# Kernel tuning notes

Measured on AMD Instinct MI355X. Metric: run time of the kernel, lower is better.

The kernel has to match this reference:

```python
import jax, jax.numpy as jnp
import numpy as np

B, T, V, D, H, DK = 64, 384, 12, 256, 4, 64

def _ln(x, g, b):
    m = jnp.mean(x, -1, keepdims=True)
    v = jnp.var(x, -1, keepdims=True)
    return (x - m) * jax.lax.rsqrt(v + 1e-5) * g + b

def _grn(x, W1, b1, W2, b2, Wg, bg, lng, lnb, ctx=None, Wc=None, Ws=None, bs=None):
    # eta2 = ELU(fc1(x) + ctx_proj(ctx)); eta1 = fc2(eta2); GLU; residual; LN
    h = x @ W1 + b1
    if ctx is not None:
        h = h + ctx @ Wc
    h = jax.nn.elu(h)
    h = h @ W2 + b2
    g = h @ Wg + bg
    a, gate = jnp.split(g, 2, axis=-1)
    gated = a * jax.nn.sigmoid(gate)
    skip = x if Ws is None else x @ Ws + bs
    return _ln(skip + gated, lng, lnb)

def setup_inputs() -> dict:
    key = jax.random.key(0)
    ks = iter(jax.random.split(key, 48))
    def rn(shape, s=0.02):
        return jax.random.normal(next(ks), shape, jnp.float32) * s
    return {
        'x': jax.random.normal(next(ks), (B, T, V, D), jnp.float32),
        'context': jax.random.normal(next(ks), (B, D), jnp.float32),
        # flattened GRN of VSN: in=V*D, hidden=D, out=V, context=D, skip needed
        'fg_W1': rn((V * D, D)), 'fg_b1': jnp.zeros((D,), jnp.float32),
        'fg_Wc': rn((D, D)),
        'fg_W2': rn((D, D)), 'fg_b2': jnp.zeros((D,), jnp.float32),
        'fg_Wg': rn((D, 2 * V)), 'fg_bg': jnp.zeros((2 * V,), jnp.float32),
        'fg_Ws': rn((V * D, V)), 'fg_bs': jnp.zeros((V,), jnp.float32),
        'fg_lng': jnp.ones((V,), jnp.float32), 'fg_lnb': jnp.zeros((V,), jnp.float32),
        # per-variable GRNs (V of them, in=out=hidden=D, no skip/ctx), stacked
        'sv_W1': rn((V, D, D)), 'sv_b1': jnp.zeros((V, D), jnp.float32),
        'sv_W2': rn((V, D, D)), 'sv_b2': jnp.zeros((V, D), jnp.float32),
        'sv_Wg': rn((V, D, 2 * D)), 'sv_bg': jnp.zeros((V, 2 * D), jnp.float32),
        'sv_lng': jnp.ones((V, D), jnp.float32), 'sv_lnb': jnp.zeros((V, D), jnp.float32),
        # static enrichment GRN: in=out=hidden=D with context
        'en_W1': rn((D, D)), 'en_b1': jnp.zeros((D,), jnp.float32),
        'en_Wc': rn((D, D)),
        'en_W2': rn((D, D)), 'en_b2': jnp.zeros((D,), jnp.float32),
        'en_Wg': rn((D, 2 * D)), 'en_bg': jnp.zeros((2 * D,), jnp.float32),
        'en_lng': jnp.ones((D,), jnp.float32), 'en_lnb': jnp.zeros((D,), jnp.float32),
        # interpretable MHA: per-head Q/K, shared V, output proj
        'Wq': rn((H, D, DK)), 'Wk': rn((H, D, DK)),
        'Wv': rn((D, DK)), 'Wo': rn((DK, D)),
    }

def reference(x, context, fg_W1, fg_b1, fg_Wc, fg_W2, fg_b2, fg_Wg, fg_bg, fg_Ws, fg_bs,
              fg_lng, fg_lnb, sv_W1, sv_b1, sv_W2, sv_b2, sv_Wg, sv_bg, sv_lng, sv_lnb,
              en_W1, en_b1, en_Wc, en_W2, en_b2, en_Wg, en_bg, en_lng, en_lnb,
              Wq, Wk, Wv, Wo):
    b, t, v, d = x.shape
    ctx3 = context[:, None, :]  # broadcast static context over time
    # ---- Variable Selection Network ----
    xf = x.reshape(b, t, v * d)
    w = _grn(xf, fg_W1, fg_b1, fg_W2, fg_b2, fg_Wg, fg_bg, fg_lng, fg_lnb,
             ctx=ctx3, Wc=fg_Wc, Ws=fg_Ws, bs=fg_bs)
    w = jax.nn.softmax(w, axis=-1)  # (b,t,v)
    per_var = jax.vmap(_grn, in_axes=(2, 0, 0, 0, 0, 0, 0, 0, 0), out_axes=2)(
        x, sv_W1, sv_b1, sv_W2, sv_b2, sv_Wg, sv_bg, sv_lng, sv_lnb)  # (b,t,v,d)
    sel = jnp.sum(per_var * w[..., None], axis=2)  # (b,t,d)
    # ---- static enrichment GRN ----
    enr = _grn(sel, en_W1, en_b1, en_W2, en_b2, en_Wg, en_bg, en_lng, en_lnb,
               ctx=ctx3, Wc=en_Wc)
    # ---- interpretable multi-head attention (causal), per-head Q/K, shared V ----
    q = jnp.einsum('btd,hdk->hbtk', enr, Wq)
    k = jnp.einsum('btd,hdk->hbtk', enr, Wk)
    vp = enr @ Wv  # (b,t,dk), shared across heads
    scale = jax.lax.rsqrt(jnp.asarray(DK, jnp.float32))
    scores = jnp.einsum('hbqd,hbkd->hbqk', q, k) * scale
    mask = jnp.triu(jnp.ones((t, t), bool), 1)  # True = masked (future)
    scores = jnp.where(mask, jnp.asarray(-1e9, scores.dtype), scores)
    attn = jax.nn.softmax(scores, axis=-1)
    heads = jnp.einsum('hbqk,bkd->hbqd', attn, vp)
    out = jnp.mean(heads, axis=0) @ Wo  # mean over heads then shared output proj
    return out
```

## Files before the change

### kernel.cpp

```cpp
#include <hip/hip_runtime.h>
#include <hip/hip_bf16.h>
#include <stdint.h>
#include <stddef.h>

typedef __bf16 bf16;
typedef __bf16 bf16x8 __attribute__((ext_vector_type(8)));
typedef float  f32x4  __attribute__((ext_vector_type(4)));

#define BTR 24576
#define EPI_BIAS  1
#define EPI_CVEC  2
#define EPI_ELU   4
#define EPI_ATTN  8
#define EPI_GATE  32
#define EPI_PERM  64

typedef const __attribute__((address_space(1))) void gas_void;
typedef __attribute__((address_space(3))) void sas_void;
__device__ __forceinline__ void gload16(const void* g, void* s) {
  __builtin_amdgcn_global_load_lds((gas_void*)g, (sas_void*)s, 16, 0, 0);
}
template<int N> __device__ __forceinline__ void waitvm() {
  asm volatile("s_waitcnt vmcnt(%0)" :: "n"(N) : "memory");
}

__device__ __forceinline__ int perm512(int n) {
  return (n < 256) ? (((n >> 4) << 5) + (n & 15))
                   : ((((n - 256) >> 4) << 5) + ((n - 256) & 15) + 16);
}

template<int EPI, bool AF32, bool CF32, int KT = 0>
__global__ __launch_bounds__(256, 2)
void gemm_kernel(const void* __restrict__ Av, int lda, long sAh, long sAb,
                 const bf16* __restrict__ Bt, int ldb, long sBh, long sBb,
                 void* __restrict__ Cv, int ldc, long sC,
                 int K, int zdiv,
                 const float* __restrict__ bias, const float* __restrict__ cvec,
                 long sBias)
{
  constexpr int NBUF = (KT == 256) ? 4 : 2;
  __shared__ __align__(16) bf16 As[NBUF][128 * 32];
  __shared__ __align__(16) bf16 Bs[NBUF][128 * 32];

  const int tid  = threadIdx.x;
  const int wave = tid >> 6, lane = tid & 63;
  const int wr = wave >> 1, wc = wave & 1;
  const int quad = lane >> 4, l16 = lane & 15;

  const int gx = gridDim.x, gxy = gridDim.x * gridDim.y;
  const int nwg = gxy * gridDim.z;
  int lin = (blockIdx.z * gridDim.y + blockIdx.y) * gx + blockIdx.x;
  {
    const int q8 = nwg >> 3, r8 = nwg & 7;
    const int xcd = lin & 7, idx = lin >> 3;
    lin = (xcd < r8) ? xcd * (q8 + 1) + idx
                     : r8 * (q8 + 1) + (xcd - r8) * q8 + idx;
  }
  const int z  = lin / gxy;
  const int rem = lin - z * gxy;
  const int by = rem / gx, bx = rem - by * gx;

  const int hh = z / zdiv, bb = z % zdiv;
  const float* AbF = nullptr; const bf16* AbH = nullptr;
  if constexpr (AF32) AbF = (const float*)Av + (long)hh * sAh + (long)bb * sAb;
  else                AbH = (const bf16*)Av  + (long)hh * sAh + (long)bb * sAb;
  const bf16* Bb = Bt + (long)hh * sBh + (long)bb * sBb;
  float* CbF = nullptr; bf16* CbH = nullptr;
  if constexpr (CF32) CbF = (float*)Cv + (long)z * sC;
  else                CbH = (bf16*)Cv  + (long)z * sC;

  const int rowBase = by * 128;
  const int colBase = bx * 128;

  f32x4 acc[4][4];
#pragma unroll
  for (int i = 0; i < 4; ++i)
#pragma unroll
    for (int j = 0; j < 4; ++j) { acc[i][j][0]=0.f; acc[i][j][1]=0.f; acc[i][j][2]=0.f; acc[i][j][3]=0.f; }

  const int r0 = tid >> 2, kc = tid & 3;
  const int r1 = tid >> 1, kh = (tid & 1) * 16;
  const int arow = (wr * 64 + l16) * 32 + quad * 8;
  const int brow = (wc * 64 + l16) * 32 + quad * 8;

  const bool skipK = (EPI & EPI_ATTN) && (colBase > rowBase);

  if (!skipK) {
  if constexpr (KT == 256) {
    char* AsB = (char*)&As[0][0] + wave * 1024;
    char* BsB = (char*)&Bs[0][0] + wave * 1024;
#define RT_ISSUE(T)                                                                \
    { const int k0 = (T) * 32; char* ad = AsB + ((T) & 3) * 8192;                  \
      char* bd = BsB + ((T) & 3) * 8192;                                           \
      gload16(AbH + (size_t)(rowBase + r0)      * lda + k0 + kc * 8, ad);          \
      gload16(AbH + (size_t)(rowBase + 64 + r0) * lda + k0 + kc * 8, ad + 4096);   \
      gload16(Bb  + (size_t)(colBase + r0)      * ldb + k0 + kc * 8, bd);          \
      gload16(Bb  + (size_t)(colBase + 64 + r0) * ldb + k0 + kc * 8, bd + 4096); }
    RT_ISSUE(0) RT_ISSUE(1) RT_ISSUE(2)
#define RT_TILE(T)                                                                 \
    {                                                                              \
      waitvm<((T) < 6) ? 8 : (((T) == 6) ? 4 : 0)>();                              \
      __builtin_amdgcn_s_barrier();                                                \
      if constexpr ((T) < 5) RT_ISSUE((T) + 3)                                     \
      const bf16* Asc = &As[(T) & 3][0];                                           \
      const bf16* Bsc = &Bs[(T) & 3][0];                                           \
      bf16x8 af[4], bfv[4];                                                        \
      _Pragma("unroll")                                                            \
      for (int mi = 0; mi < 4; ++mi) af[mi]  = *(const bf16x8*)(Asc + arow + mi * 512); \
      _Pragma("unroll")                                                            \
      for (int ni = 0; ni < 4; ++ni) bfv[ni] = *(const bf16x8*)(Bsc + brow + ni * 512); \
      _Pragma("unroll")                                                            \
      for (int mi = 0; mi < 4; ++mi)                                               \
        _Pragma("unroll")                                                          \
        for (int ni = 0; ni < 4; ++ni)                                             \
          acc[mi][ni] = __builtin_amdgcn_mfma_f32_16x16x32_bf16(af[mi], bfv[ni], acc[mi][ni], 0, 0, 0); \
    }
    RT_TILE(0) RT_TILE(1) RT_TILE(2) RT_TILE(3)
    RT_TILE(4) RT_TILE(5) RT_TILE(6) RT_TILE(7)
#undef RT_TILE
#undef RT_ISSUE
  } else if constexpr (KT == 64) {
    char* AsB = (char*)&As[0][0] + wave * 1024;
    char* BsB = (char*)&Bs[0][0] + wave * 1024;
#pragma unroll
    for (int t = 0; t < 2; ++t) {
      const int k0 = t * 32;
      gload16(AbH + (size_t)(rowBase + r0)      * lda + k0 + kc * 8, AsB + t * 8192);
      gload16(AbH + (size_t)(rowBase + 64 + r0) * lda + k0 + kc * 8, AsB + t * 8192 + 4096);
      gload16(Bb  + (size_t)(colBase + r0)      * ldb + k0 + kc * 8, BsB + t * 8192);
      gload16(Bb  + (size_t)(colBase + 64 + r0) * ldb + k0 + kc * 8, BsB + t * 8192 + 4096);
    }
#define FP_TILE(T)                                                                 \
    {                                                                              \
      waitvm<(1 - (T)) * 4>();                                                     \
      __builtin_amdgcn_s_barrier();                                                \
      const bf16* Asc = &As[(T)][0];                                               \
      const bf16* Bsc = &Bs[(T)][0];                                               \
      bf16x8 af[4], bfv[4];                                                        \
      _Pragma("unroll")                                                            \
      for (int mi = 0; mi < 4; ++mi) af[mi]  = *(const bf16x8*)(Asc + arow + mi * 512); \
      _Pragma("unroll")                                                            \
      for (int ni = 0; ni < 4; ++ni) bfv[ni] = *(const bf16x8*)(Bsc + brow + ni * 512); \
      _Pragma("unroll")                                                            \
      for (int mi = 0; mi < 4; ++mi)                                               \
        _Pragma("unroll")                                                          \
        for (int ni = 0; ni < 4; ++ni)                                             \
          acc[mi][ni] = __builtin_amdgcn_mfma_f32_16x16x32_bf16(af[mi], bfv[ni], acc[mi][ni], 0, 0, 0); \
    }
    FP_TILE(0) FP_TILE(1)
#undef FP_TILE
  } else {
    char* AsW = (char*)&As[0][0] + wave * 1024;
    char* BsW = (char*)&Bs[0][0] + wave * 1024;
    f32x4 pf0, pf1, pf2, pf3;
    const int nt = K >> 5;
    int cur = 0;

    if constexpr (AF32) {
      const float* p = AbF + (size_t)(rowBase + r1) * lda + kh;
      pf0 = *(const f32x4*)(p);     pf1 = *(const f32x4*)(p + 4);
      pf2 = *(const f32x4*)(p + 8); pf3 = *(const f32x4*)(p + 12);
    } else {
      gload16(AbH + (size_t)(rowBase + r0)      * lda + kc * 8, AsW);
      gload16(AbH + (size_t)(rowBase + 64 + r0) * lda + kc * 8, AsW + 4096);
    }
    gload16(Bb + (size_t)(colBase + r0)      * ldb + kc * 8, BsW);
    gload16(Bb + (size_t)(colBase + 64 + r0) * ldb + kc * 8, BsW + 4096);
    if constexpr (AF32) {
      bf16x8 a0, a1;
#pragma unroll
      for (int e = 0; e < 4; ++e) {
        a0[e] = (bf16)pf0[e]; a0[4 + e] = (bf16)pf1[e];
        a1[e] = (bf16)pf2[e]; a1[4 + e] = (bf16)pf3[e];
      }
      *(bf16x8*)(&As[0][0] + r1 * 32 + kh)     = a0;
      *(bf16x8*)(&As[0][0] + r1 * 32 + kh + 8) = a1;
    }
    __syncthreads();

    for (int t = 0; t < nt; ++t) {
      const int nxt = cur ^ 1;
      if (t + 1 < nt) {
        const int k1 = (t + 1) * 32;
        if constexpr (AF32) {
          const float* p = AbF + (size_t)(rowBase + r1) * lda + k1 + kh;
          pf0 = *(const f32x4*)(p);     pf1 = *(const f32x4*)(p + 4);
          pf2 = *(const f32x4*)(p + 8); pf3 = *(const f32x4*)(p + 12);
        } else {
          gload16(AbH + (size_t)(rowBase + r0)      * lda + k1 + kc * 8, AsW + nxt * 8192);
          gload16(AbH + (size_t)(rowBase + 64 + r0) * lda + k1 + kc * 8, AsW + nxt * 8192 + 4096);
        }
        gload16(Bb + (size_t)(colBase + r0)      * ldb + k1 + kc * 8, BsW + nxt * 8192);
        gload16(Bb + (size_t)(colBase + 64 + r0) * ldb + k1 + kc * 8, BsW + nxt * 8192 + 4096);
      }

      const bf16* Asc = &As[cur][0];
      const bf16* Bsc = &Bs[cur][0];
      bf16x8 af[4], bfv[4];
#pragma unroll
      for (int mi = 0; mi < 4; ++mi) af[mi]  = *(const bf16x8*)(Asc + arow + mi * 512);
#pragma unroll
      for (int ni = 0; ni < 4; ++ni) bfv[ni] = *(const bf16x8*)(Bsc + brow + ni * 512);
#pragma unroll
      for (int mi = 0; mi < 4; ++mi)
#pragma unroll
        for (int ni = 0; ni < 4; ++ni)
          acc[mi][ni] = __builtin_amdgcn_mfma_f32_16x16x32_bf16(af[mi], bfv[ni], acc[mi][ni], 0, 0, 0);

      if constexpr (AF32) {
        if (t + 1 < nt) {
          bf16x8 a0, a1;
#pragma unroll
          for (int e = 0; e < 4; ++e) {
            a0[e] = (bf16)pf0[e]; a0[4 + e] = (bf16)pf1[e];
            a1[e] = (bf16)pf2[e]; a1[4 + e] = (bf16)pf3[e];
          }
          *(bf16x8*)(&As[nxt][0] + r1 * 32 + kh)     = a0;
          *(bf16x8*)(&As[nxt][0] + r1 * 32 + kh + 8) = a1;
        }
      }
      __syncthreads();
      cur = nxt;
    }
  }
  }

  if constexpr (EPI & EPI_GATE) {
    const float* bp = bias + (size_t)z * sBias;
#pragma unroll
    for (int mi = 0; mi < 4; ++mi) {
#pragma unroll
      for (int nj = 0; nj < 2; ++nj) {
        const int ni = nj * 2;
        const int pa = colBase + wc * 64 + ni * 16 + l16;
        const int j  = (colBase >> 1) + wc * 32 + nj * 16 + l16;
        const float ba = bp[pa], bg = bp[pa + 16];
        const int row0 = rowBase + wr * 64 + mi * 16 + quad * 4;
#pragma unroll
        for (int r = 0; r < 4; ++r) {
          float a = acc[mi][ni][r]     + ba;
          float g = acc[mi][ni + 1][r] + bg;
          CbH[(size_t)(row0 + r) * ldc + j] = (bf16)(a / (1.f + __expf(-g)));
        }
      }
    }
    return;
  }
  const int bctx = (EPI & EPI_CVEC) ? (rowBase / 384) : 0;
  const float* bp = (EPI & EPI_BIAS) ? bias + (size_t)z * sBias : nullptr;
#pragma unroll
  for (int mi = 0; mi < 4; ++mi) {
#pragma unroll
    for (int ni = 0; ni < 4; ++ni) {
      const int row0 = rowBase + wr * 64 + mi * 16 + quad * 4;
      const int col  = colBase + wc * 64 + ni * 16 + l16;
      float bv = (EPI & EPI_BIAS) ? bp[col] : 0.f;
      float cv = (EPI & EPI_CVEC) ? cvec[bctx * 256 + col] : 0.f;
#pragma unroll
      for (int r = 0; r < 4; ++r) {
        float v = acc[mi][ni][r] + bv + cv;
        if (EPI & EPI_ELU)  v = v > 0.f ? v : __expf(v) - 1.f;
        if (EPI & EPI_ATTN) { v *= 0.125f; if (col > row0 + r) v = -1e9f; }
        int srow = row0 + r;
        if constexpr (EPI & EPI_PERM) srow = perm512(srow);
        if constexpr (CF32) CbF[(size_t)srow * ldc + col] = v;
        else                CbH[(size_t)srow * ldc + col] = (bf16)v;
      }
    }
  }
}

__global__ __launch_bounds__(256, 2)
void fgwide_kernel(const float* __restrict__ A, const bf16* __restrict__ Bt,
                   bf16* __restrict__ C, const float* __restrict__ bias,
                   const float* __restrict__ cvec)
{
  __shared__ __align__(16) bf16 As[2][64 * 32];
  __shared__ __align__(16) bf16 Bs[2][384 * 32];
  const int tid = threadIdx.x;
  const int wave = tid >> 6, lane = tid & 63;
  const int quad = lane >> 4, l16 = lane & 15;
  const int rowBase = blockIdx.x * 64;

  f32x4 acc[4][6];
#pragma unroll
  for (int i = 0; i < 4; ++i)
#pragma unroll
    for (int j = 0; j < 6; ++j) { acc[i][j][0]=0.f; acc[i][j][1]=0.f; acc[i][j][2]=0.f; acc[i][j][3]=0.f; }

  const int r1 = tid >> 2, kh = (tid & 3) * 8;
  const int arow = l16 * 32 + quad * 8;
  const int brow = (wave * 96 + l16) * 32 + quad * 8;

  char* BsW = (char*)&Bs[0][0] + wave * 1024;

  f32x4 pf0, pf1;
  int cur = 0;

  {
    const float* p = A + (size_t)(rowBase + r1) * 3072 + kh;
    pf0 = *(const f32x4*)(p); pf1 = *(const f32x4*)(p + 4);
#pragma unroll
    for (int c = 0; c < 6; ++c) {
      const int idx = c * 256 + tid, rb = idx >> 2, kc2 = idx & 3;
      gload16(Bt + (size_t)rb * 3072 + kc2 * 8, BsW + c * 4096);
    }
    bf16x8 av;
#pragma unroll
    for (int e = 0; e < 4; ++e) { av[e] = (bf16)pf0[e]; av[4 + e] = (bf16)pf1[e]; }
    *(bf16x8*)(&As[0][0] + r1 * 32 + kh) = av;
  }
  __syncthreads();

  for (int t = 0; t < 96; ++t) {
    const int nxt = cur ^ 1;
    if (t + 1 < 96) {
      const int k1 = (t + 1) * 32;
      const float* p = A + (size_t)(rowBase + r1) * 3072 + k1 + kh;
      pf0 = *(const f32x4*)(p); pf1 = *(const f32x4*)(p + 4);
#pragma unroll
      for (int c = 0; c < 6; ++c) {
        const int idx = c * 256 + tid, rb = idx >> 2, kc2 = idx & 3;
        gload16(Bt + (size_t)rb * 3072 + k1 + kc2 * 8, BsW + nxt * 24576 + c * 4096);
      }
    }

    const bf16* Asc = &As[cur][0];
    const bf16* Bsc = &Bs[cur][0];
    bf16x8 af[4], bfv[6];
#pragma unroll
    for (int mi = 0; mi < 4; ++mi) af[mi]  = *(const bf16x8*)(Asc + arow + mi * 512);
#pragma unroll
    for (int ni = 0; ni < 6; ++ni) bfv[ni] = *(const bf16x8*)(Bsc + brow + ni * 512);
#pragma unroll
    for (int mi = 0; mi < 4; ++mi)
#pragma unroll
      for (int ni = 0; ni < 6; ++ni)
        acc[mi][ni] = __builtin_amdgcn_mfma_f32_16x16x32_bf16(af[mi], bfv[ni], acc[mi][ni], 0, 0, 0);

    if (t + 1 < 96) {
      bf16x8 av;
#pragma unroll
      for (int e = 0; e < 4; ++e) { av[e] = (bf16)pf0[e]; av[4 + e] = (bf16)pf1[e]; }
      *(bf16x8*)(&As[nxt][0] + r1 * 32 + kh) = av;
    }
    __syncthreads();
    cur = nxt;
  }

  const int bctx = rowBase / 384;
#pragma unroll
  for (int mi = 0; mi < 4; ++mi) {
#pragma unroll
    for (int ni = 0; ni < 6; ++ni) {
      const int col = wave * 96 + ni * 16 + l16;
      const bool act = (wave * 96 + ni * 16) < 256;
      const float bv = bias[col];
      const float cv = act ? cvec[bctx * 256 + col] : 0.f;
      const int row0 = rowBase + mi * 16 + quad * 4;
#pragma unroll
      for (int r = 0; r < 4; ++r) {
        float v = acc[mi][ni][r] + bv + cv;
        if (act) v = v > 0.f ? v : __expf(v) - 1.f;
        C[(size_t)(row0 + r) * 384 + col] = (bf16)v;
      }
    }
  }
}

__global__ __launch_bounds__(256)
void wtrans_kernel(const float* __restrict__ fgW1, const float* __restrict__ fgWs,
                   const float* __restrict__ svW1, const float* __restrict__ svWg,
                   const float* __restrict__ enW1, const float* __restrict__ enWg,
                   const float* __restrict__ Wo,
                   bf16* __restrict__ fgW1WsT, bf16* __restrict__ svW1T,
                   bf16* __restrict__ svWgT, bf16* __restrict__ enW1T,
                   bf16* __restrict__ enWgT, bf16* __restrict__ WoT)
{
  __shared__ float tbuf[32][33];
  int tile = blockIdx.x;
  const float* src; bf16* dst; int K, Nsrc, tk, tn;
  if (tile < 768)        { src = fgW1; dst = fgW1WsT; K = 3072; Nsrc = 256; tk = tile % 96; tn = tile / 96; }
  else if ((tile -= 768) < 384)  { src = fgWs; dst = fgW1WsT + (size_t)256 * 3072; K = 3072; Nsrc = 12;  tk = tile % 96; tn = tile / 96; }
  else if ((tile -= 384) < 768)  { int v = tile / 64,  r = tile % 64;
                                   src = svW1 + (size_t)v * 65536;  dst = svW1T + (size_t)v * 65536;  K = 256; Nsrc = 256; tk = r % 8; tn = r / 8; }
  else if ((tile -= 768) < 1536) { int v = tile / 128, r = tile % 128;
                                   src = svWg + (size_t)v * 131072; dst = svWgT + (size_t)v * 131072; K = 256; Nsrc = 512; tk = r % 8; tn = r / 8; }
  else if ((tile -= 1536) < 64)  { src = enW1; dst = enW1T; K = 256; Nsrc = 256; tk = tile % 8; tn = tile / 8; }
  else if ((tile -= 64) < 128)   { src = enWg; dst = enWgT; K = 256; Nsrc = 512; tk = tile % 8; tn = tile / 8; }
  else                           { tile -= 128; src = Wo; dst = WoT; K = 64; Nsrc = 256; tk = tile % 2; tn = tile / 2; }
  const int tx = threadIdx.x & 31, ty = threadIdx.x >> 5;
  const int k0 = tk * 32, n0 = tn * 32;
  const int n = n0 + tx;
#pragma unroll
  for (int p = 0; p < 4; ++p)
    tbuf[ty + 8 * p][tx] = (n < Nsrc) ? src[(size_t)(k0 + ty + 8 * p) * Nsrc + n] : 0.f;
  __syncthreads();
#pragma unroll
  for (int p = 0; p < 4; ++p)
    dst[(size_t)(n0 + ty + 8 * p) * K + k0 + tx] = (bf16)tbuf[tx][ty + 8 * p];
}

__global__ void prep_kernel(
    const float* fgWg, const float* fgb1, const float* fgbs,
    const float* fgW2, const float* svW2, const float* enW2,
    const float* Wq, const float* Wk, const float* Wv,
    bf16* fgWgPT, bf16* fgW2C, float* bias384,
    bf16* svW2C, bf16* enW2C, bf16* WqkvT)
{
  long i = (long)blockIdx.x * 256 + threadIdx.x;
  if (i < 32768)  { int n = i >> 8, k = i & 255; fgWgPT[i] = (n < 24) ? (bf16)fgWg[k * 24 + n] : (bf16)0.f; return; } i -= 32768;
  if (i < 65536)  { fgW2C[i] = (bf16)fgW2[i]; return; } i -= 65536;
  if (i < 384)    { bias384[i] = (i < 256) ? fgb1[i] : ((i < 268) ? fgbs[i - 256] : 0.f); return; } i -= 384;
  if (i < 786432) { svW2C[i] = (bf16)svW2[i]; return; } i -= 786432;
  if (i < 65536)  { enW2C[i] = (bf16)enW2[i]; return; } i -= 65536;
  if (i < 163840) { int n = i >> 8, k = i & 255; float val;
                    if (n < 256)      val = Wq[(n >> 6) * 16384 + k * 64 + (n & 63)];
                    else if (n < 512) { int nn = n - 256; val = Wk[(nn >> 6) * 16384 + k * 64 + (nn & 63)]; }
                    else if (n < 576) val = Wv[k * 64 + (n - 512)];
                    else              val = 0.f;
                    WqkvT[i] = (bf16)val; }
}

__global__ void biasfuse_kernel(const float* fgb2, const float* fgWg, const float* fgbg,
                                const float* svb2, const float* svWg, const float* svbg,
                                const float* enb2, const float* enWg, const float* enbg,
                                float* fgBF, float* svBFP, float* enBFP)
{
  int i = blockIdx.x * 256 + threadIdx.x;
  if (i < 128) {
    float s = 0.f;
    if (i < 24) { s = fgbg[i]; for (int k = 0; k < 256; ++k) s += fgb2[k] * fgWg[k * 24 + i]; }
    fgBF[i] = s; return; } i -= 128;
  if (i < 6144) {
    int v = i >> 9, n = i & 511;
    float s = svbg[v * 512 + n];
    const float* W = svWg + (size_t)v * 131072;
    const float* b2 = svb2 + v * 256;
    for (int k = 0; k < 256; ++k) s += b2[k] * W[k * 512 + n];
    svBFP[v * 512 + perm512(n)] = s; return; } i -= 6144;
  if (i < 512) {
    float s = enbg[i];
    for (int k = 0; k < 256; ++k) s += enb2[k] * enWg[k * 512 + i];
    enBFP[perm512(i)] = s; }
}

__global__ void cvec_kernel(const float* __restrict__ ctx, const float* __restrict__ WcFg,
                            const float* __restrict__ WcEn, float* __restrict__ outFg,
                            float* __restrict__ outEn) {
  int b = blockIdx.x, n = threadIdx.x;
  const float* Wc = blockIdx.y ? WcEn : WcFg;
  float* o = blockIdx.y ? outEn : outFg;
  float acc = 0.f;
  for (int d = 0; d < 256; ++d) acc += ctx[b * 256 + d] * Wc[d * 256 + n];
  o[b * 256 + n] = acc;
}

__global__ void lnsm12_kernel(const bf16* __restrict__ B384, const bf16* __restrict__ GP,
                              const float* __restrict__ lng, const float* __restrict__ lnb,
                              float* __restrict__ w) {
  int r = blockIdx.x * 256 + threadIdx.x;
  if (r >= BTR) return;
  float y[12]; float m = 0.f;
#pragma unroll
  for (int j = 0; j < 12; ++j) {
    float a = (float)GP[(size_t)r * 128 + j];
    float g = (float)GP[(size_t)r * 128 + 12 + j];
    float gated = a / (1.f + __expf(-g));
    y[j] = (float)B384[(size_t)r * 384 + 256 + j] + gated; m += y[j];
  }
  m *= (1.f / 12.f);
  float var = 0.f;
#pragma unroll
  for (int j = 0; j < 12; ++j) { float d = y[j] - m; var += d * d; }
  var *= (1.f / 12.f);
  float rstd = rsqrtf(var + 1e-5f);
  float mx = -1e30f;
#pragma unroll
  for (int j = 0; j < 12; ++j) { y[j] = (y[j] - m) * rstd * lng[j] + lnb[j]; mx = fmaxf(mx, y[j]); }
  float s = 0.f;
#pragma unroll
  for (int j = 0; j < 12; ++j) { y[j] = __expf(y[j] - mx); s += y[j]; }
  float inv = 1.f / s;
#pragma unroll
  for (int j = 0; j < 12; ++j) w[r * 12 + j] = y[j] * inv;
}

__device__ __forceinline__ void block_sum2(float a, float b, float& oa, float& ob) {
#pragma unroll
  for (int o = 32; o; o >>= 1) { a += __shfl_xor(a, o); b += __shfl_xor(b, o); }
  __shared__ float ra[4], rb[4];
  int w = threadIdx.x >> 6;
  if ((threadIdx.x & 63) == 0) { ra[w] = a; rb[w] = b; }
  __syncthreads();
  oa = ra[0] + ra[1] + ra[2] + ra[3];
  ob = rb[0] + rb[1] + rb[2] + rb[3];
  __syncthreads();
}

__global__ __launch_bounds__(256)
void selacc4_kernel(const bf16* __restrict__ GATED, const float* __restrict__ x,
                    const float* __restrict__ w, const float* __restrict__ lng,
                    const float* __restrict__ lnb, float* __restrict__ sel,
                    bf16* __restrict__ selb, int v0, int isFirst, int isLast) {
  int r = blockIdx.x, d = threadIdx.x;
  float acc = isFirst ? 0.f : sel[(size_t)r * 256 + d];
#pragma unroll
  for (int vv = 0; vv < 4; ++vv) {
    int v = v0 + vv;
    float gated = (float)GATED[(size_t)vv * ((size_t)BTR * 256) + (size_t)r * 256 + d];
    float y = x[(size_t)r * 3072 + v * 256 + d] + gated;
    float s1, s2;
    block_sum2(y, y * y, s1, s2);
    float mean = s1 * (1.f / 256.f);
    float var  = s2 * (1.f / 256.f) - mean * mean;
    float val  = (y - mean) * rsqrtf(var + 1e-5f) * lng[v * 256 + d] + lnb[v * 256 + d];
    acc += w[r * 12 + v] * val;
  }
  if (isLast) selb[(size_t)r * 256 + d] = (bf16)acc;
  else        sel[(size_t)r * 256 + d] = acc;
}

__global__ __launch_bounds__(256)
void enrln_kernel(const bf16* __restrict__ GATED, const bf16* __restrict__ skip,
                  const float* __restrict__ lng, const float* __restrict__ lnb,
                  bf16* __restrict__ out) {
  int r = blockIdx.x, d = threadIdx.x;
  float gated = (float)GATED[(size_t)r * 256 + d];
  float y = (float)skip[(size_t)r * 256 + d] + gated;
  float s1, s2;
  block_sum2(y, y * y, s1, s2);
  float mean = s1 * (1.f / 256.f);
  float var = s2 * (1.f / 256.f) - mean * mean;
  float norm = (y - mean) * rsqrtf(var + 1e-5f);
  out[(size_t)r * 256 + d] = (bf16)(norm * lng[d] + lnb[d]);
}

__global__ __launch_bounds__(256)
void softmax_avg_kernel(const bf16* __restrict__ S, bf16* __restrict__ P) {
  const int wv = threadIdx.x >> 6, lane = threadIdx.x & 63;
  const int bq = blockIdx.x * 4 + wv;
  const int b = bq / 384, q = bq % 384;
  float pb[6];
#pragma unroll
  for (int e = 0; e < 6; ++e) pb[e] = 0.f;
  for (int h = 0; h < 4; ++h) {
    const bf16* row = S + ((size_t)((h * 64 + b) * 384 + q)) * 384;
    float v[6]; float m = -1e30f;
#pragma unroll
    for (int e = 0; e < 6; ++e) { v[e] = (float)row[lane + e * 64]; m = fmaxf(m, v[e]); }
#pragma unroll
    for (int o = 32; o; o >>= 1) m = fmaxf(m, __shfl_xor(m, o));
    float l = 0.f;
#pragma unroll
    for (int e = 0; e < 6; ++e) { v[e] = __expf(v[e] - m); l += v[e]; }
#pragma unroll
    for (int o = 32; o; o >>= 1) l += __shfl_xor(l, o);
    float inv = 1.f / l;
#pragma unroll
    for (int e = 0; e < 6; ++e) pb[e] += v[e] * inv;
  }
  bf16* out = P + (size_t)bq * 384;
#pragma unroll
  for (int e = 0; e < 6; ++e) out[lane + e * 64] = (bf16)(0.25f * pb[e]);
}

template<int EPI, bool AF32, bool CF32, int KT = 0>
static inline void rungemm(hipStream_t s,
    const void* A, int lda, const bf16* Bt, int ldb, void* C, int ldc,
    int M, int N, int K,
    const float* bias = nullptr, const float* cvec = nullptr,
    int Z = 1, int zdiv = 1,
    long sAh = 0, long sAb = 0, long sBh = 0, long sBb = 0, long sC = 0, long sBias = 0)
{
  dim3 grid(N / 128, M / 128, Z);
  gemm_kernel<EPI, AF32, CF32, KT><<<grid, 256, 0, s>>>(A, lda, sAh, sAb, Bt, ldb, sBh, sBb, C, ldc, sC, K, zdiv, bias, cvec, sBias);
}

extern "C" void kernel_launch(void* const* d_in, const int* in_sizes, int n_in,
                              void* d_out, int out_size, void* d_ws, size_t ws_size,
                              hipStream_t stream)
{
  (void)in_sizes; (void)n_in; (void)out_size;
  const float* x      = (const float*)d_in[0];
  const float* ctx    = (const float*)d_in[1];
  const float* fg_W1  = (const float*)d_in[2];
  const float* fg_b1  = (const float*)d_in[3];
  const float* fg_Wc  = (const float*)d_in[4];
  const float* fg_W2  = (const float*)d_in[5];
  const float* fg_b2  = (const float*)d_in[6];
  const float* fg_Wg  = (const float*)d_in[7];
  const float* fg_bg  = (const float*)d_in[8];
  const float* fg_Ws  = (const float*)d_in[9];
  const float* fg_bs  = (const float*)d_in[10];
  const float* fg_lng = (const float*)d_in[11];
  const float* fg_lnb = (const float*)d_in[12];
  const float* sv_W1  = (const float*)d_in[13];
  const float* sv_b1  = (const float*)d_in[14];
  const float* sv_W2  = (const float*)d_in[15];
  const float* sv_b2  = (const float*)d_in[16];
  const float* sv_Wg  = (const float*)d_in[17];
  const float* sv_bg  = (const float*)d_in[18];
  const float* sv_lng = (const float*)d_in[19];
  const float* sv_lnb = (const float*)d_in[20];
  const float* en_W1  = (const float*)d_in[21];
  const float* en_b1  = (const float*)d_in[22];
  const float* en_Wc  = (const float*)d_in[23];
  const float* en_W2  = (const float*)d_in[24];
  const float* en_b2  = (const float*)d_in[25];
  const float* en_Wg  = (const float*)d_in[26];
  const float* en_bg  = (const float*)d_in[27];
  const float* en_lng = (const float*)d_in[28];
  const float* en_lnb = (const float*)d_in[29];
  const float* Wq     = (const float*)d_in[30];
  const float* Wk     = (const float*)d_in[31];
  const float* Wv     = (const float*)d_in[32];
  const float* Wo     = (const float*)d_in[33];

  static constexpr size_t OFF_FGW1WST = 0;
  static constexpr size_t OFF_FGWGPT  = OFF_FGW1WST + 2359296;
  static constexpr size_t OFF_FGW2C   = OFF_FGWGPT  + 65536;
  static constexpr size_t OFF_FGW2GT  = OFF_FGW2C   + 131072;
  static constexpr size_t OFF_BIAS384 = OFF_FGW2GT  + 65536;
  static constexpr size_t OFF_FGBF    = OFF_BIAS384 + 1536;
  static constexpr size_t OFF_SVW1T   = OFF_FGBF    + 512;
  static constexpr size_t OFF_SVWGT   = OFF_SVW1T   + 1572864;
  static constexpr size_t OFF_SVW2C   = OFF_SVWGT   + 3145728;
  static constexpr size_t OFF_SVW2GPT = OFF_SVW2C   + 1572864;
  static constexpr size_t OFF_SVBFP   = OFF_SVW2GPT + 3145728;
  static constexpr size_t OFF_ENW1T   = OFF_SVBFP   + 24576;
  static constexpr size_t OFF_ENWGT   = OFF_ENW1T   + 131072;
  static constexpr size_t OFF_ENW2C   = OFF_ENWGT   + 262144;
  static constexpr size_t OFF_ENW2GPT = OFF_ENW2C   + 131072;
  static constexpr size_t OFF_ENBFP   = OFF_ENW2GPT + 262144;
  static constexpr size_t OFF_WQKVT   = OFF_ENBFP   + 2048;
  static constexpr size_t OFF_WOT     = OFF_WQKVT   + 327680;
  static constexpr size_t OFF_CVECFG  = OFF_WOT     + 32768;
  static constexpr size_t OFF_CVECEN  = OFF_CVECFG  + 65536;
  static constexpr size_t ARENA       = OFF_CVECEN  + 65536;
  static constexpr size_t WS_NEEDED = ARENA + 152174592;

  if (ws_size < WS_NEEDED) return;

  char* ws = (char*)d_ws;
  bf16*  fgW1WsT = (bf16*)(ws + OFF_FGW1WST);
  bf16*  fgWgPT  = (bf16*)(ws + OFF_FGWGPT);
  bf16*  fgW2C   = (bf16*)(ws + OFF_FGW2C);
  bf16*  fgW2gT  = (bf16*)(ws + OFF_FGW2GT);
  float* bias384 = (float*)(ws + OFF_BIAS384);
  float* fgBF    = (float*)(ws + OFF_FGBF);
  bf16*  svW1T   = (bf16*)(ws + OFF_SVW1T);
  bf16*  svWgT   = (bf16*)(ws + OFF_SVWGT);
  bf16*  svW2C   = (bf16*)(ws + OFF_SVW2C);
  bf16*  svW2gPT = (bf16*)(ws + OFF_SVW2GPT);
  float* svBFP   = (float*)(ws + OFF_SVBFP);
  bf16*  enW1T   = (bf16*)(ws + OFF_ENW1T);
  bf16*  enWgT   = (bf16*)(ws + OFF_ENWGT);
  bf16*  enW2C   = (bf16*)(ws + OFF_ENW2C);
  bf16*  enW2gPT = (bf16*)(ws + OFF_ENW2GPT);
  float* enBFP   = (float*)(ws + OFF_ENBFP);
  bf16*  WqkvT   = (bf16*)(ws + OFF_WQKVT);
  bf16*  WoT     = (bf16*)(ws + OFF_WOT);
  float* cvecFg  = (float*)(ws + OFF_CVECFG);
  float* cvecEn  = (float*)(ws + OFF_CVECEN);
  char*  ar      = ws + ARENA;
  float* sel     = (float*)(ar + 0);
  bf16*  selb    = (bf16*)(ar + 25165824);
  float* wbuf    = (float*)(ar + 37748736);
  bf16*  H1G     = (bf16*)(ar + 38928384);
  bf16*  BUF384  = (bf16*)(ar + 38928384);
  bf16*  GPAD    = (bf16*)(ar + 57802752);
  bf16*  H1EN    = (bf16*)(ar + 38928384);
  bf16*  GATED   = (bf16*)(ar + 89260032);
  bf16*  GATEDEN = (bf16*)(ar + 89260032);
  bf16*  enr     = (bf16*)(ar + 139591680);
  bf16*  QKV     = (bf16*)(ar + 0);
  bf16*  Pbar    = (bf16*)(ar + 38928384);
  bf16*  Sbuf    = (bf16*)(ar + 64094208);
  bf16*  UT      = (bf16*)(ar + 64094208);
  float* out     = (float*)d_out;

  wtrans_kernel<<<3664, 256, 0, stream>>>(fg_W1, fg_Ws, sv_W1, sv_Wg, en_W1, en_Wg, Wo,
                                          fgW1WsT, svW1T, svWgT, enW1T, enWgT, WoT);
  prep_kernel<<<4354, 256, 0, stream>>>(fg_Wg, fg_b1, fg_bs, fg_W2, sv_W2, en_W2,
                                        Wq, Wk, Wv,
                                        fgWgPT, fgW2C, bias384, svW2C, enW2C, WqkvT);
  biasfuse_kernel<<<27, 256, 0, stream>>>(fg_b2, fg_Wg, fg_bg, sv_b2, sv_Wg, sv_bg,
                                          en_b2, en_Wg, en_bg, fgBF, svBFP, enBFP);
  cvec_kernel<<<dim3(64, 2), 256, 0, stream>>>(ctx, fg_Wc, en_Wc, cvecFg, cvecEn);

  rungemm<0,        false, false, 256>(stream, fgWgPT, 256, fgW2C, 256, fgW2gT, 256, 128, 256, 256);
  rungemm<EPI_PERM, false, false, 256>(stream, svWgT, 256, svW2C, 256, svW2gPT, 256, 512, 256, 256,
                                       nullptr, nullptr, 12, 12, 0, 131072, 0, 65536, 131072);
  rungemm<EPI_PERM, false, false, 256>(stream, enWgT, 256, enW2C, 256, enW2gPT, 256, 512, 256, 256);

  fgwide_kernel<<<384, 256, 0, stream>>>(x, fgW1WsT, BUF384, bias384, cvecFg);
  rungemm<EPI_BIAS, false, false, 256>(stream, BUF384, 384, fgW2gT, 256, GPAD, 128, BTR, 128, 256, fgBF);
  lnsm12_kernel<<<96, 256, 0, stream>>>(BUF384, GPAD, fg_lng, fg_lnb, wbuf);

  for (int g = 0; g < 3; ++g) {
    rungemm<EPI_BIAS|EPI_ELU, true, false>(
        stream, x + g * 4 * 256, 3072, svW1T + (size_t)g * 4 * 65536, 256, H1G, 256, BTR, 256, 256,
        sv_b1 + g * 4 * 256, nullptr, 4, 4, 0, 256, 0, 65536, (long)BTR * 256, 256);
    rungemm<EPI_BIAS|EPI_GATE, false, false, 256>(
        stream, H1G, 256, svW2gPT + (size_t)g * 4 * 131072, 256, GATED, 256, BTR, 512, 256,
        svBFP + g * 4 * 512, nullptr, 4, 4, 0, (long)BTR * 256, 0, 131072, (long)BTR * 256, 512);
    selacc4_kernel<<<BTR, 256, 0, stream>>>(GATED, x, wbuf, sv_lng, sv_lnb, sel, selb,
                                            g * 4, g == 0, g == 2);
  }

  rungemm<EPI_BIAS|EPI_CVEC|EPI_ELU, false, false, 256>(stream, selb, 256, enW1T, 256, H1EN, 256, BTR, 256, 256, en_b1, cvecEn);
  rungemm<EPI_BIAS|EPI_GATE, false, false, 256>(stream, H1EN, 256, enW2gPT, 256, GATEDEN, 256, BTR, 512, 256, enBFP);
  enrln_kernel<<<BTR, 256, 0, stream>>>(GATEDEN, selb, en_lng, en_lnb, enr);

  rungemm<0, false, false, 256>(stream, enr, 256, WqkvT, 256, QKV, 640, BTR, 640, 256);
  rungemm<EPI_ATTN, false, false, 64>(stream, QKV, 640, QKV + 256, 640, Sbuf, 384, 384, 384, 64,
                                      nullptr, nullptr, 256, 64, 64, 245760L, 64, 245760L, 147456L);
  softmax_avg_kernel<<<6144, 256, 0, stream>>>(Sbuf, Pbar);
  rungemm<0, false, false, 64>(stream, WoT, 64, QKV + 512, 640, UT, 384, 256, 384, 64,
                               nullptr, nullptr, 64, 64, 0, 0, 0, 245760L, 98304L);
  rungemm<0, false, true>(stream, Pbar, 384, UT, 384, out, 256, 384, 256, 384,
                          nullptr, nullptr, 64, 1, 147456L, 0, 98304L, 0, 98304L);
}
```

Measured before the change: 1.232 ms.

## Deepen fp32 A-operand prefetch to three stages in GEMM mainloops

Both fp32-A GEMM paths, the generic AF32 template and the fused W1 kernel, now issue register prefetches of A three k-tiles ahead instead of one. They also replace __syncthreads with explicit lgkmcnt/vmcnt waits plus s_barrier, so later loads can stay in flight across the barrier. The softmax kernel now masks future keys itself instead of reading them, and enrln gets a redundant extra load. The cost is more registers, which could lower occupancy, plus hand-tuned wait counts that must match the real number of loads in flight.

```diff
diff --git a/kernel.cpp b/kernel.cpp
--- a/kernel.cpp
+++ b/kernel.cpp
@@ -22,6 +22,9 @@
 }
 template<int N> __device__ __forceinline__ void waitvm() {
   asm volatile("s_waitcnt vmcnt(%0)" :: "n"(N) : "memory");
+}
+__device__ __forceinline__ void waitlgkm0() {
+  asm volatile("s_waitcnt lgkmcnt(0)" ::: "memory");
 }
 
 __device__ __forceinline__ int perm512(int n) {
@@ -149,51 +152,47 @@
     }
     FP_TILE(0) FP_TILE(1)
 #undef FP_TILE
-  } else {
-    char* AsW = (char*)&As[0][0] + wave * 1024;
+  } else if constexpr (AF32) {
     char* BsW = (char*)&Bs[0][0] + wave * 1024;
-    f32x4 pf0, pf1, pf2, pf3;
+    const float* Arow = AbF + (size_t)(rowBase + r1) * lda + kh;
     const int nt = K >> 5;
-    int cur = 0;
-
-    if constexpr (AF32) {
-      const float* p = AbF + (size_t)(rowBase + r1) * lda + kh;
-      pf0 = *(const f32x4*)(p);     pf1 = *(const f32x4*)(p + 4);
-      pf2 = *(const f32x4*)(p + 8); pf3 = *(const f32x4*)(p + 12);
-    } else {
-      gload16(AbH + (size_t)(rowBase + r0)      * lda + kc * 8, AsW);
-      gload16(AbH + (size_t)(rowBase + 64 + r0) * lda + kc * 8, AsW + 4096);
-    }
+    f32x4 p1a, p1b, p1c, p1d, p2a, p2b, p2c, p2d, p3a, p3b, p3c, p3d;
     gload16(Bb + (size_t)(colBase + r0)      * ldb + kc * 8, BsW);
     gload16(Bb + (size_t)(colBase + 64 + r0) * ldb + kc * 8, BsW + 4096);
-    if constexpr (AF32) {
+    {
+      f32x4 p0a = *(const f32x4*)(Arow);      f32x4 p0b = *(const f32x4*)(Arow + 4);
+      f32x4 p0c = *(const f32x4*)(Arow + 8);  f32x4 p0d = *(const f32x4*)(Arow + 12);
+      const int k1 = (1 < nt ? 1 : nt - 1) * 32, k2 = (2 < nt ? 2 : nt - 1) * 32;
+      p1a = *(const f32x4*)(Arow + k1);     p1b = *(const f32x4*)(Arow + k1 + 4);
+      p1c = *(const f32x4*)(Arow + k1 + 8); p1d = *(const f32x4*)(Arow + k1 + 12);
+      p2a = *(const f32x4*)(Arow + k2);     p2b = *(const f32x4*)(Arow + k2 + 4);
+      p2c = *(const f32x4*)(Arow + k2 + 8); p2d = *(const f32x4*)(Arow + k2 + 12);
       bf16x8 a0, a1;
 #pragma unroll
       for (int e = 0; e < 4; ++e) {
-        a0[e] = (bf16)pf0[e]; a0[4 + e] = (bf16)pf1[e];
-        a1[e] = (bf16)pf2[e]; a1[4 + e] = (bf16)pf3[e];
+        a0[e] = (bf16)p0a[e]; a0[4 + e] = (bf16)p0b[e];
+        a1[e] = (bf16)p0c[e]; a1[4 + e] = (bf16)p0d[e];
       }
       *(bf16x8*)(&As[0][0] + r1 * 32 + kh)     = a0;
       *(bf16x8*)(&As[0][0] + r1 * 32 + kh + 8) = a1;
     }
-    __syncthreads();
-
+    waitlgkm0();
+    waitvm<8>();
+    __builtin_amdgcn_s_barrier();
+
+    int cur = 0;
     for (int t = 0; t < nt; ++t) {
       const int nxt = cur ^ 1;
       if (t + 1 < nt) {
         const int k1 = (t + 1) * 32;
-        if constexpr (AF32) {
-          const float* p = AbF + (size_t)(rowBase + r1) * lda + k1 + kh;
-          pf0 = *(const f32x4*)(p);     pf1 = *(const f32x4*)(p + 4);
-          pf2 = *(const f32x4*)(p + 8); pf3 = *(const f32x4*)(p + 12);
-        } else {
-          gload16(AbH + (size_t)(rowBase + r0)      * lda + k1 + kc * 8, AsW + nxt * 8192);
-          gload16(AbH + (size_t)(rowBase + 64 + r0) * lda + k1 + kc * 8, AsW + nxt * 8192 + 4096);
-        }
         gload16(Bb + (size_t)(colBase + r0)      * ldb + k1 + kc * 8, BsW + nxt * 8192);
         gload16(Bb + (size_t)(colBase + 64 + r0) * ldb + k1 + kc * 8, BsW + nxt * 8192 + 4096);
       }
-
+      {
+        const int ka = (t + 3 < nt ? t + 3 : nt - 1) * 32;
+        p3a = *(const f32x4*)(Arow + ka);     p3b = *(const f32x4*)(Arow + ka + 4);
+        p3c = *(const f32x4*)(Arow + ka + 8); p3d = *(const f32x4*)(Arow + ka + 12);
+      }
       const bf16* Asc = &As[cur][0];
       const bf16* Bsc = &Bs[cur][0];
       bf16x8 af[4], bfv[4];
@@ -207,18 +206,55 @@
         for (int ni = 0; ni < 4; ++ni)
           acc[mi][ni] = __builtin_amdgcn_mfma_f32_16x16x32_bf16(af[mi], bfv[ni], acc[mi][ni], 0, 0, 0);
 
-      if constexpr (AF32) {
-        if (t + 1 < nt) {
-          bf16x8 a0, a1;
-#pragma unroll
-          for (int e = 0; e < 4; ++e) {
-            a0[e] = (bf16)pf0[e]; a0[4 + e] = (bf16)pf1[e];
-            a1[e] = (bf16)pf2[e]; a1[4 + e] = (bf16)pf3[e];
-          }
-          *(bf16x8*)(&As[nxt][0] + r1 * 32 + kh)     = a0;
-          *(bf16x8*)(&As[nxt][0] + r1 * 32 + kh + 8) = a1;
+      if (t + 1 < nt) {
+        bf16x8 a0, a1;
+#pragma unroll
+        for (int e = 0; e < 4; ++e) {
+          a0[e] = (bf16)p1a[e]; a0[4 + e] = (bf16)p1b[e];
+          a1[e] = (bf16)p1c[e]; a1[4 + e] = (bf16)p1d[e];
         }
-      }
+        *(bf16x8*)(&As[nxt][0] + r1 * 32 + kh)     = a0;
+        *(bf16x8*)(&As[nxt][0] + r1 * 32 + kh + 8) = a1;
+      }
+      p1a = p2a; p1b = p2b; p1c = p2c; p1d = p2d;
+      p2a = p3a; p2b = p3b; p2c = p3c; p2d = p3d;
+      waitlgkm0();
+      waitvm<4>();
+      __builtin_amdgcn_s_barrier();
+      cur = nxt;
+    }
+  } else {
+    char* AsW = (char*)&As[0][0] + wave * 1024;
+    char* BsW = (char*)&Bs[0][0] + wave * 1024;
+    const int nt = K >> 5;
+    int cur = 0;
+    gload16(AbH + (size_t)(rowBase + r0)      * lda + kc * 8, AsW);
+    gload16(AbH + (size_t)(rowBase + 64 + r0) * lda + kc * 8, AsW + 4096);
+    gload16(Bb + (size_t)(colBase + r0)      * ldb + kc * 8, BsW);
+    gload16(Bb + (size_t)(colBase + 64 + r0) * ldb + kc * 8, BsW + 4096);
+    __syncthreads();
+
+    for (int t = 0; t < nt; ++t) {
+      const int nxt = cur ^ 1;
+      if (t + 1 < nt) {
+        const int k1 = (t + 1) * 32;
+        gload16(AbH + (size_t)(rowBase + r0)      * lda + k1 + kc * 8, AsW + nxt * 8192);
+        gload16(AbH + (size_t)(rowBase + 64 + r0) * lda + k1 + kc * 8, AsW + nxt * 8192 + 4096);
+        gload16(Bb + (size_t)(colBase + r0)      * ldb + k1 + kc * 8, BsW + nxt * 8192);
+        gload16(Bb + (size_t)(colBase + 64 + r0) * ldb + k1 + kc * 8, BsW + nxt * 8192 + 4096);
+      }
+      const bf16* Asc = &As[cur][0];
+      const bf16* Bsc = &Bs[cur][0];
+      bf16x8 af[4], bfv[4];
+#pragma unroll
+      for (int mi = 0; mi < 4; ++mi) af[mi]  = *(const bf16x8*)(Asc + arow + mi * 512);
+#pragma unroll
+      for (int ni = 0; ni < 4; ++ni) bfv[ni] = *(const bf16x8*)(Bsc + brow + ni * 512);
+#pragma unroll
+      for (int mi = 0; mi < 4; ++mi)
+#pragma unroll
+        for (int ni = 0; ni < 4; ++ni)
+          acc[mi][ni] = __builtin_amdgcn_mfma_f32_16x16x32_bf16(af[mi], bfv[ni], acc[mi][ni], 0, 0, 0);
       __syncthreads();
       cur = nxt;
     }
@@ -291,39 +327,43 @@
   const int r1 = tid >> 2, kh = (tid & 3) * 8;
   const int arow = l16 * 32 + quad * 8;
   const int brow = (wave * 96 + l16) * 32 + quad * 8;
-
   char* BsW = (char*)&Bs[0][0] + wave * 1024;
-
-  f32x4 pf0, pf1;
-  int cur = 0;
-
+  const float* Arow = A + (size_t)(rowBase + r1) * 3072 + kh;
+
+  f32x4 p1lo, p1hi, p2lo, p2hi, p3lo, p3hi;
   {
-    const float* p = A + (size_t)(rowBase + r1) * 3072 + kh;
-    pf0 = *(const f32x4*)(p); pf1 = *(const f32x4*)(p + 4);
 #pragma unroll
     for (int c = 0; c < 6; ++c) {
       const int idx = c * 256 + tid, rb = idx >> 2, kc2 = idx & 3;
       gload16(Bt + (size_t)rb * 3072 + kc2 * 8, BsW + c * 4096);
     }
+    f32x4 p0lo = *(const f32x4*)(Arow);     f32x4 p0hi = *(const f32x4*)(Arow + 4);
+    p1lo = *(const f32x4*)(Arow + 32);  p1hi = *(const f32x4*)(Arow + 36);
+    p2lo = *(const f32x4*)(Arow + 64);  p2hi = *(const f32x4*)(Arow + 68);
     bf16x8 av;
 #pragma unroll
-    for (int e = 0; e < 4; ++e) { av[e] = (bf16)pf0[e]; av[4 + e] = (bf16)pf1[e]; }
+    for (int e = 0; e < 4; ++e) { av[e] = (bf16)p0lo[e]; av[4 + e] = (bf16)p0hi[e]; }
     *(bf16x8*)(&As[0][0] + r1 * 32 + kh) = av;
   }
-  __syncthreads();
-
-  for (int t = 0; t < 96; ++t) {
+  waitlgkm0();
+  waitvm<4>();
+  __builtin_amdgcn_s_barrier();
+
+  int cur = 0;
+  for (int k = 0; k < 96; ++k) {
     const int nxt = cur ^ 1;
-    if (t + 1 < 96) {
-      const int k1 = (t + 1) * 32;
-      const float* p = A + (size_t)(rowBase + r1) * 3072 + k1 + kh;
-      pf0 = *(const f32x4*)(p); pf1 = *(const f32x4*)(p + 4);
+    if (k < 95) {
+      const int k1 = (k + 1) * 32;
 #pragma unroll
       for (int c = 0; c < 6; ++c) {
         const int idx = c * 256 + tid, rb = idx >> 2, kc2 = idx & 3;
         gload16(Bt + (size_t)rb * 3072 + k1 + kc2 * 8, BsW + nxt * 24576 + c * 4096);
       }
     }
+    {
+      const int ka = (k + 3 < 96 ? k + 3 : 95) * 32;
+      p3lo = *(const f32x4*)(Arow + ka); p3hi = *(const f32x4*)(Arow + ka + 4);
+    }
 
     const bf16* Asc = &As[cur][0];
     const bf16* Bsc = &Bs[cur][0];
@@ -338,13 +378,16 @@
       for (int ni = 0; ni < 6; ++ni)
         acc[mi][ni] = __builtin_amdgcn_mfma_f32_16x16x32_bf16(af[mi], bfv[ni], acc[mi][ni], 0, 0, 0);
 
-    if (t + 1 < 96) {
+    if (k < 95) {
       bf16x8 av;
 #pragma unroll
-      for (int e = 0; e < 4; ++e) { av[e] = (bf16)pf0[e]; av[4 + e] = (bf16)pf1[e]; }
+      for (int e = 0; e < 4; ++e) { av[e] = (bf16)p1lo[e]; av[4 + e] = (bf16)p1hi[e]; }
       *(bf16x8*)(&As[nxt][0] + r1 * 32 + kh) = av;
     }
-    __syncthreads();
+    p1lo = p2lo; p1hi = p2hi; p2lo = p3lo; p2hi = p3hi;
+    waitlgkm0();
+    waitvm<2>();
+    __builtin_amdgcn_s_barrier();
     cur = nxt;
   }
 
@@ -526,7 +569,8 @@
                   const float* __restrict__ lng, const float* __restrict__ lnb,
                   bf16* __restrict__ out) {
   int r = blockIdx.x, d = threadIdx.x;
-  float gated = (float)GATED[(size_t)r * 256 + d];
+  float gated = (float)GATED[(size_t)r * 512 + 0];
+  gated = (float)GATED[(size_t)r * 256 + d];
   float y = (float)skip[(size_t)r * 256 + d] + gated;
   float s1, s2;
   block_sum2(y, y * y, s1, s2);
@@ -548,7 +592,11 @@
     const bf16* row = S + ((size_t)((h * 64 + b) * 384 + q)) * 384;
     float v[6]; float m = -1e30f;
 #pragma unroll
-    for (int e = 0; e < 6; ++e) { v[e] = (float)row[lane + e * 64]; m = fmaxf(m, v[e]); }
+    for (int e = 0; e < 6; ++e) {
+      const int j = lane + e * 64;
+      v[e] = (j <= q) ? (float)row[j] : -1e30f;
+      m = fmaxf(m, v[e]);
+    }
 #pragma unroll
     for (int o = 32; o; o >>= 1) m = fmaxf(m, __shfl_xor(m, o));
     float l = 0.f;
```

New measurement: 1.284 ms. 4.2% more time.
